# Optimization experiments

Hardware: AMD Instinct MI355X
Metric: run time of the kernel (lower is better)

## Reference

```python
import jax, jax.numpy as jnp
import numpy as np

XY = 16   # xy_size
Z = 16    # z_size
S = XY * XY * Z   # num_states = 4096
V = 2048  # num_tokens


def _build_structure():
    # Static 3D-grid neighbor structure (replaces the per-state Python loop).
    h = np.arange(S)
    zc, rem = np.divmod(h, XY * XY)
    yc, xc = np.divmod(rem, XY)
    coords = np.stack([xc, yc, zc], 1)                       # [S,3] (x,y,z)
    offs = np.array([[0, 0, 0], [1, 0, 0], [-1, 0, 0], [0, 1, 0],
                     [0, -1, 0], [0, 0, 1], [0, 0, 2]])       # 7 fixed offsets
    nc = coords[:, None, :] + offs[None]                      # [S,7,3]
    valid = ((nc[..., 0] >= 0) & (nc[..., 0] < XY) &
             (nc[..., 1] >= 0) & (nc[..., 1] < XY) &
             (nc[..., 2] >= 0) & (nc[..., 2] < Z))
    dest = nc[..., 0] + XY * (nc[..., 1] + XY * nc[..., 2])   # flat neighbor idx
    # compact valid neighbors to the front, preserving offset order:
    # j-th valid neighbor consumes logit j (matches logits[h, :len(valid)])
    order = np.argsort(~valid, axis=1, kind='stable')
    tgt = np.take_along_axis(dest, order, axis=1)
    vmask = np.take_along_axis(valid, order, axis=1)
    tgt = np.where(vmask, tgt, S)  # invalid slots -> dummy column S
    return jnp.asarray(tgt), jnp.asarray(vmask)

TGT, VMASK = _build_structure()


def transition_log_p(trans_w):
    # masked log-softmax over the first k valid logits of each row
    logits = jnp.where(VMASK, trans_w, -1e30)
    logp = jax.nn.log_softmax(logits, axis=1)
    logp = jnp.where(VMASK, logp, -jnp.inf)
    T = jnp.full((S, S + 1), -jnp.inf, trans_w.dtype)
    T = T.at[jnp.arange(S)[:, None], TGT].set(logp)
    return T[:, :S]  # [S,S], row h = log p(transition targets of h)


def smoothed_emission(emis_w):
    em = jax.nn.log_softmax(emis_w, axis=-1).reshape(Z, XY, XY, V)
    lv, rv = em[:, :, :1], em[:, :, -1:]
    lh, rh = em[:, :1], em[:, -1:]
    c = jnp.zeros((Z, 1, 1, V), em.dtype)  # log(1)=0 pad, as in the original
    c2 = lambda *a: jnp.concatenate(a, axis=2)
    c1 = lambda *a: jnp.concatenate(a, axis=1)
    up = c1(c2(lv, em, rv), c2(c, rh, c), c2(c, rh, c))
    dn = c1(c2(c, lh, c), c2(c, lh, c), c2(lv, em, rv))
    lf = c1(c2(lh, c, c), c2(em, rv, rv), c2(rh, c, c))
    rt = c1(c2(c, c, lh), c2(lv, lv, em), c2(c, c, rh))
    cr = c1(c2(c, lh, c), c2(lv, em, rv), c2(c, rh, c))
    mean = jax.nn.logsumexp(jnp.stack((up, dn, lf, rt, cr)), axis=0) - jnp.log(5.0)
    return mean[:, 1:-1, 1:-1].reshape(S, V)


def _forward(stories, trans_w, emis_w, prior_w):
    priors = jax.nn.log_softmax(prior_w)                      # [S]
    em = smoothed_emission(emis_w)                            # [S,V]
    padded = jnp.concatenate([em, jnp.zeros((S, 1), em.dtype)], axis=1)  # [S,V+1]
    # per-(story, step) emission log-prob: sum over sentence tokens
    all_emis = padded.T[stories].sum(axis=2)                  # [B,L,S]
    all_emis = jnp.transpose(all_emis, (1, 0, 2))             # [L,B,S]
    T = transition_log_p(trans_w)                             # [S,S]
    amax = jnp.max(T, axis=1, keepdims=True)                  # [S,1], finite (self-loop)
    P = jnp.exp(T - amax)                                     # [S,S]
    score0 = all_emis[0] + priors                             # [B,S]

    def step(score, em_t):
        # new[b,a] = em_t[b,a] + logsumexp_h(T[a,h] + score[b,h])  (stable log-matmul)
        smax = jnp.max(score, axis=1, keepdims=True)          # [B,1]
        new = em_t + jnp.log(jnp.exp(score - smax) @ P.T) + smax + amax.T
        return new, new

    _, rest = jax.lax.scan(step, score0, all_emis[1:])
    return jnp.concatenate([score0[None], rest], axis=0)      # [L,B,S]


def setup_inputs() -> dict:
    key = jax.random.key(0)
    k1, k2, k3, k4 = jax.random.split(key, 4)
    B, L, W = 8, 32, 8
    return {
        "stories_tensor": jax.random.randint(k1, (B, L, W), 0, V + 1, dtype=jnp.int32),
        "story_length": L,
        "trans_w": jax.random.normal(k2, (S, 7), jnp.float32),
        "emis_w": jax.random.normal(k3, (S, V), jnp.float32),
        "prior_w": jax.random.normal(k4, (S,), jnp.float32),
    }


def reference(stories_tensor, story_length, trans_w, emis_w, prior_w):
    assert stories_tensor.shape[1] == story_length
    return _forward(stories_tensor, trans_w, emis_w, prior_w)
```

## Files before the change

kernel.cpp:

```cpp
#include <hip/hip_runtime.h>
#include <math.h>

#define XYD 16
#define ZD 16
#define SS 4096
#define VV 2048
#define BB 8
#define LL 32
#define WW 8
#define VC 32
#define SM_STRIDE 257

#define GUARD_L 16
#define GUARD_R 512
#define EBUF_N (GUARD_L + SS + GUARD_R)

__global__ void k_logZ(const float* __restrict__ emis_w, float* __restrict__ logZ) {
    int wave = threadIdx.x >> 6;
    int lane = threadIdx.x & 63;
    int row  = blockIdx.x * 4 + wave;
    const float* r = emis_w + (size_t)row * VV;
    float vals[32];
    float m = -INFINITY;
#pragma unroll
    for (int k = 0; k < 8; k++) {
        float4 f = ((const float4*)r)[k * 64 + lane];
        vals[k*4+0] = f.x; vals[k*4+1] = f.y; vals[k*4+2] = f.z; vals[k*4+3] = f.w;
    }
#pragma unroll
    for (int k = 0; k < 32; k++) m = fmaxf(m, vals[k]);
#pragma unroll
    for (int o = 32; o; o >>= 1) m = fmaxf(m, __shfl_xor(m, o));
    float sum = 0.f;
#pragma unroll
    for (int k = 0; k < 32; k++) sum += __expf(vals[k] - m);
#pragma unroll
    for (int o = 32; o; o >>= 1) sum += __shfl_xor(sum, o);
    if (lane == 0) logZ[row] = m + __logf(sum);
}

__global__ void k_smooth(const float* __restrict__ emis_w, const float* __restrict__ logZ,
                         float* __restrict__ smT) {
    __shared__ float tileT[VC * SM_STRIDE];
    int z  = blockIdx.x;
    int v0 = blockIdx.y * VC;
    int tid = threadIdx.x;
    int rsub = tid >> 3;
    int c0   = (tid & 7) * 4;

#pragma unroll
    for (int it = 0; it < 8; it++) {
        int r  = it * 32 + rsub;
        int sg = z * 256 + r;
        float lz = logZ[sg];
        float4 w = *(const float4*)(emis_w + (size_t)sg * VV + v0 + c0);
        tileT[(c0+0)*SM_STRIDE + r] = __expf(w.x - lz);
        tileT[(c0+1)*SM_STRIDE + r] = __expf(w.y - lz);
        tileT[(c0+2)*SM_STRIDE + r] = __expf(w.z - lz);
        tileT[(c0+3)*SM_STRIDE + r] = __expf(w.w - lz);
    }
    __syncthreads();

    int x = tid & 15, y = tid >> 4;
    int sxp = (x < 15) ? tid + 1  : tid;
    int sxm = (x > 0)  ? tid - 1  : tid;
    int syp = (y < 15) ? tid + 16 : tid;
    int sym = (y > 0)  ? tid - 16 : tid;
    float* o = smT + (size_t)v0 * SS + z * 256 + tid;
#pragma unroll
    for (int i = 0; i < VC; i++) {
        const float* tb = tileT + i * SM_STRIDE;
        float s = tb[tid] + tb[sxp] + tb[sxm] + tb[syp] + tb[sym];
        o[(size_t)i * SS] = __logf(s * 0.2f);
    }
}

__global__ void k_emis(const int* __restrict__ stories, const float* __restrict__ smT,
                       float* __restrict__ all_emis) {
    int blk = blockIdx.x;
    int t = blk >> 3, b = blk & 7;
    int tid = threadIdx.x;
    int tok[WW];
#pragma unroll
    for (int w = 0; w < WW; w++) tok[w] = stories[(b * LL + t) * WW + w];
#pragma unroll
    for (int i = 0; i < 4; i++) {
        int s = i * 1024 + tid * 4;
        float4 acc = {0.f, 0.f, 0.f, 0.f};
#pragma unroll
        for (int w = 0; w < WW; w++) {
            if (tok[w] < VV) {
                float4 f = *(const float4*)(smT + (size_t)tok[w] * SS + s);
                acc.x += f.x; acc.y += f.y; acc.z += f.z; acc.w += f.w;
            }
        }
        *(float4*)(all_emis + ((size_t)t * BB + b) * SS + s) = acc;
    }
}

__global__ void __launch_bounds__(1024) k_forward(
    const float* __restrict__ trans_w, const float* __restrict__ prior_w,
    const float* __restrict__ all_emis, float* __restrict__ out) {
    __shared__ __align__(16) float Ebuf[2][EBUF_N];
    __shared__ float red2[2][20];
    __shared__ float pr[16];
    int b = blockIdx.x;
    int tid = threadIdx.x;
    int lane = tid & 63, wid = tid >> 6;

    if (tid < GUARD_L) { Ebuf[0][tid] = 0.f; Ebuf[1][tid] = 0.f; }
    if (tid < GUARD_R) {
        Ebuf[0][GUARD_L + SS + tid] = 0.f;
        Ebuf[1][GUARD_L + SS + tid] = 0.f;
    }
    if (tid < 2) {
        red2[tid][0]  = -INFINITY; red2[tid][17] = -INFINITY;
        red2[tid][18] = -INFINITY; red2[tid][19] = -INFINITY;
    }

    float pw[28], am[4];
    {
        float w7[28];
        const float4* t4 = (const float4*)(trans_w + (size_t)tid * 28);
#pragma unroll
        for (int k = 0; k < 7; k++) ((float4*)w7)[k] = t4[k];
#pragma unroll
        for (int i = 0; i < 4; i++) {
            int j = tid * 4 + i;
            int xx = j & 15, yy = (j >> 4) & 15, zz = j >> 8;
            bool val[7];
            val[0] = true;
            val[1] = (xx < 15); val[2] = (xx > 0);
            val[3] = (yy < 15); val[4] = (yy > 0);
            val[5] = (zz < 15); val[6] = (zz < 14);
            const float* rw = w7 + i * 7;
            float w[7]; int cnt = 0; float m = -INFINITY;
#pragma unroll
            for (int d = 0; d < 7; d++) { if (val[d]) { w[d] = rw[cnt++]; m = fmaxf(m, w[d]); } }
            float se = 0.f;
#pragma unroll
            for (int d = 0; d < 7; d++) if (val[d]) se += __expf(w[d] - m);
#pragma unroll
            for (int d = 0; d < 7; d++) pw[i*7+d] = val[d] ? __expf(w[d] - m) : 0.f;
            am[i] = -__logf(se);
        }
    }

    float4 pv = ((const float4*)prior_w)[tid];
    float4 em = ((const float4*)(all_emis + (size_t)b * SS))[tid];

    float lm = fmaxf(fmaxf(pv.x, pv.y), fmaxf(pv.z, pv.w));
#pragma unroll
    for (int o = 32; o; o >>= 1) lm = fmaxf(lm, __shfl_xor(lm, o));
    if (lane == 0) pr[wid] = lm;
    __syncthreads();
    float gm = pr[0];
#pragma unroll
    for (int w = 1; w < 16; w++) gm = fmaxf(gm, pr[w]);
    __syncthreads();
    float ls = __expf(pv.x - gm) + __expf(pv.y - gm) + __expf(pv.z - gm) + __expf(pv.w - gm);
#pragma unroll
    for (int o = 32; o; o >>= 1) ls += __shfl_xor(ls, o);
    if (lane == 0) pr[wid] = ls;
    __syncthreads();
    float gs = 0.f;
#pragma unroll
    for (int w = 0; w < 16; w++) gs += pr[w];
    float logZp = gm + __logf(gs);

    float v0 = em.x + pv.x - logZp;
    float v1 = em.y + pv.y - logZp;
    float v2 = em.z + pv.z - logZp;
    float v3 = em.w + pv.w - logZp;
    { float4 ov = {v0, v1, v2, v3}; ((float4*)(out + (size_t)b * SS))[tid] = ov; }
    float c = fmaxf(fmaxf(v0, v1), fmaxf(v2, v3));
#pragma unroll
    for (int o = 32; o; o >>= 1) c = fmaxf(c, __shfl_xor(c, o));
    float4 Ereg;
    Ereg.x = __expf(v0 - c); Ereg.y = __expf(v1 - c);
    Ereg.z = __expf(v2 - c); Ereg.w = __expf(v3 - c);
    ((float4*)(Ebuf[0] + GUARD_L))[tid] = Ereg;
    if (lane == 0) red2[0][1 + wid] = c;

    float4 em_next = ((const float4*)(all_emis + (size_t)BB * SS + (size_t)b * SS))[tid];

    int cur = 0;
    for (int t = 1; t < LL; t++) {
        __syncthreads();
        em = em_next;
        if (t < LL - 1)
            em_next = ((const float4*)(all_emis + ((size_t)(t + 1) * BB + b) * SS))[tid];

        const float* rr = red2[cur];
        float c_m1 = rr[wid], c0f = rr[wid + 1], c1f = rr[wid + 2], c2f = rr[wid + 3];
        bool lo = (lane < 4);
        float X = fmaxf(fmaxf(c0f, c1f), c2f);
        if (lo) X = fmaxf(X, c_m1);
        float f0 = __expf(c0f - X), f1 = __expf(c1f - X), f2 = __expf(c2f - X);
        float fm1 = lo ? __expf(c_m1 - X) : 0.f;

        const float*  Es = Ebuf[cur] + GUARD_L;
        const float4* Ep = (const float4*)Es;
        float  bx  = Es[4 * tid + 4];
        float  cxw = Es[4 * tid - 1];
        float4 Yp = Ep[tid + 4];
        float4 Ym = Ep[tid - 4];
        float4 Zp = Ep[tid + 64];
        float4 Zq = Ep[tid + 128];

        float4 Af;
        Af.x = Ereg.x * f0; Af.y = Ereg.y * f0; Af.z = Ereg.z * f0; Af.w = Ereg.w * f0;
        bx  *= (lane == 63) ? f1 : f0;
        cxw *= (lane == 0)  ? fm1 : f0;
        float fyp = (lane >= 60) ? f1 : f0;
        float fym = lo ? fm1 : f0;
        Yp.x *= fyp; Yp.y *= fyp; Yp.z *= fyp; Yp.w *= fyp;
        Ym.x *= fym; Ym.y *= fym; Ym.z *= fym; Ym.w *= fym;
        Zp.x *= f1;  Zp.y *= f1;  Zp.z *= f1;  Zp.w *= f1;
        Zq.x *= f2;  Zq.y *= f2;  Zq.z *= f2;  Zq.w *= f2;

        float a0 = Af.x*pw[0]  + Af.y*pw[1]  + cxw*pw[2]   + Yp.x*pw[3]  + Ym.x*pw[4]  + Zp.x*pw[5]  + Zq.x*pw[6];
        float a1 = Af.y*pw[7]  + Af.z*pw[8]  + Af.x*pw[9]  + Yp.y*pw[10] + Ym.y*pw[11] + Zp.y*pw[12] + Zq.y*pw[13];
        float a2 = Af.z*pw[14] + Af.w*pw[15] + Af.y*pw[16] + Yp.z*pw[17] + Ym.z*pw[18] + Zp.z*pw[19] + Zq.z*pw[20];
        float a3 = Af.w*pw[21] + bx*pw[22]   + Af.z*pw[23] + Yp.w*pw[24] + Ym.w*pw[25] + Zp.w*pw[26] + Zq.w*pw[27];

        v0 = em.x + __logf(a0) + X + am[0];
        v1 = em.y + __logf(a1) + X + am[1];
        v2 = em.z + __logf(a2) + X + am[2];
        v3 = em.w + __logf(a3) + X + am[3];

        { float4 ov = {v0, v1, v2, v3};
          ((float4*)(out + ((size_t)t * BB + b) * SS))[tid] = ov; }

        c = fmaxf(fmaxf(v0, v1), fmaxf(v2, v3));
#pragma unroll
        for (int o = 32; o; o >>= 1) c = fmaxf(c, __shfl_xor(c, o));
        Ereg.x = __expf(v0 - c); Ereg.y = __expf(v1 - c);
        Ereg.z = __expf(v2 - c); Ereg.w = __expf(v3 - c);
        ((float4*)(Ebuf[cur ^ 1] + GUARD_L))[tid] = Ereg;
        if (lane == 0) red2[cur ^ 1][1 + wid] = c;

        cur ^= 1;
    }
}

extern "C" void kernel_launch(void* const* d_in, const int* in_sizes, int n_in,
                              void* d_out, int out_size, void* d_ws, size_t ws_size,
                              hipStream_t stream) {
    const int*   stories = (const int*)d_in[0];
    const float* trans_w = (const float*)d_in[2];
    const float* emis_w  = (const float*)d_in[3];
    const float* prior_w = (const float*)d_in[4];
    float* out = (float*)d_out;

    char* ws = (char*)d_ws;
    float* smT      = (float*)(ws);
    float* all_emis = (float*)(ws + (size_t)VV * SS * 4);
    float* logZ     = (float*)(ws + (size_t)VV * SS * 4 + (size_t)LL * BB * SS * 4);

    k_logZ<<<SS / 4, 256, 0, stream>>>(emis_w, logZ);
    k_smooth<<<dim3(ZD, VV / VC), 256, 0, stream>>>(emis_w, logZ, smT);
    k_emis<<<LL * BB, 256, 0, stream>>>(stories, smT, all_emis);
    k_forward<<<BB, 1024, 0, stream>>>(trans_w, prior_w, all_emis, out);
}
```

Measured before the change: 167.1 us.

## Store forward exp-buffer in bf16 and replace per-wave max with extrapolated shift

The recursion's shared exp buffer now holds bf16 values instead of fp32, which halves LDS traffic for the stencil neighbour loads. The per-wave max reduction (shuffles plus cross-wave rescale factors) is dropped. Each step instead uses a single scalar shift: state 0's score, linearly extrapolated from the previous two steps. This removes several shuffles, exps and multiplies from the serial per-step critical path. The costs are bf16 truncation error and possible overflow or underflow of exp when other states drift far from state 0's score.

```diff
diff --git a/kernel.cpp b/kernel.cpp
--- a/kernel.cpp
+++ b/kernel.cpp
@@ -15,6 +15,13 @@
 #define GUARD_R 512
 #define EBUF_N (GUARD_L + SS + GUARD_R)
 
+__device__ __forceinline__ float b2f(unsigned short u) {
+    union { unsigned int i; float f; } x; x.i = ((unsigned int)u) << 16; return x.f;
+}
+__device__ __forceinline__ unsigned short f2b(float f) {
+    union { float f; unsigned int i; } x; x.f = f; return (unsigned short)(x.i >> 16);
+}
+
 __global__ void k_logZ(const float* __restrict__ emis_w, float* __restrict__ logZ) {
     int wave = threadIdx.x >> 6;
     int lane = threadIdx.x & 63;
@@ -101,21 +108,17 @@
 __global__ void __launch_bounds__(1024) k_forward(
     const float* __restrict__ trans_w, const float* __restrict__ prior_w,
     const float* __restrict__ all_emis, float* __restrict__ out) {
-    __shared__ __align__(16) float Ebuf[2][EBUF_N];
-    __shared__ float red2[2][20];
+    __shared__ __align__(16) unsigned short Ebuf[2][EBUF_N];
+    __shared__ float red2[2];
     __shared__ float pr[16];
     int b = blockIdx.x;
     int tid = threadIdx.x;
     int lane = tid & 63, wid = tid >> 6;
 
-    if (tid < GUARD_L) { Ebuf[0][tid] = 0.f; Ebuf[1][tid] = 0.f; }
+    if (tid < GUARD_L) { Ebuf[0][tid] = 0; Ebuf[1][tid] = 0; }
     if (tid < GUARD_R) {
-        Ebuf[0][GUARD_L + SS + tid] = 0.f;
-        Ebuf[1][GUARD_L + SS + tid] = 0.f;
-    }
-    if (tid < 2) {
-        red2[tid][0]  = -INFINITY; red2[tid][17] = -INFINITY;
-        red2[tid][18] = -INFINITY; red2[tid][19] = -INFINITY;
+        Ebuf[0][GUARD_L + SS + tid] = 0;
+        Ebuf[1][GUARD_L + SS + tid] = 0;
     }
 
     float pw[28], am[4];
@@ -173,14 +176,18 @@
     float v2 = em.z + pv.z - logZp;
     float v3 = em.w + pv.w - logZp;
     { float4 ov = {v0, v1, v2, v3}; ((float4*)(out + (size_t)b * SS))[tid] = ov; }
-    float c = fmaxf(fmaxf(v0, v1), fmaxf(v2, v3));
-#pragma unroll
-    for (int o = 32; o; o >>= 1) c = fmaxf(c, __shfl_xor(c, o));
-    float4 Ereg;
-    Ereg.x = __expf(v0 - c); Ereg.y = __expf(v1 - c);
-    Ereg.z = __expf(v2 - c); Ereg.w = __expf(v3 - c);
-    ((float4*)(Ebuf[0] + GUARD_L))[tid] = Ereg;
-    if (lane == 0) red2[0][1 + wid] = c;
+    if (tid == 0) red2[0] = v0;
+    __syncthreads();
+    float g1 = red2[0];
+    float XpPrev = g1;
+    {
+        ushort4 E;
+        E.x = f2b(__expf(v0 - XpPrev)); E.y = f2b(__expf(v1 - XpPrev));
+        E.z = f2b(__expf(v2 - XpPrev)); E.w = f2b(__expf(v3 - XpPrev));
+        *(ushort4*)(&Ebuf[0][GUARD_L + 4 * tid]) = E;
+    }
+    float Erx = __expf(v0 - XpPrev), Ery = __expf(v1 - XpPrev);
+    float Erz = __expf(v2 - XpPrev), Erw = __expf(v3 - XpPrev);
 
     float4 em_next = ((const float4*)(all_emis + (size_t)BB * SS + (size_t)b * SS))[tid];
 
@@ -191,56 +198,40 @@
         if (t < LL - 1)
             em_next = ((const float4*)(all_emis + ((size_t)(t + 1) * BB + b) * SS))[tid];
 
-        const float* rr = red2[cur];
-        float c_m1 = rr[wid], c0f = rr[wid + 1], c1f = rr[wid + 2], c2f = rr[wid + 3];
-        bool lo = (lane < 4);
-        float X = fmaxf(fmaxf(c0f, c1f), c2f);
-        if (lo) X = fmaxf(X, c_m1);
-        float f0 = __expf(c0f - X), f1 = __expf(c1f - X), f2 = __expf(c2f - X);
-        float fm1 = lo ? __expf(c_m1 - X) : 0.f;
-
-        const float*  Es = Ebuf[cur] + GUARD_L;
-        const float4* Ep = (const float4*)Es;
-        float  bx  = Es[4 * tid + 4];
-        float  cxw = Es[4 * tid - 1];
-        float4 Yp = Ep[tid + 4];
-        float4 Ym = Ep[tid - 4];
-        float4 Zp = Ep[tid + 64];
-        float4 Zq = Ep[tid + 128];
-
-        float4 Af;
-        Af.x = Ereg.x * f0; Af.y = Ereg.y * f0; Af.z = Ereg.z * f0; Af.w = Ereg.w * f0;
-        bx  *= (lane == 63) ? f1 : f0;
-        cxw *= (lane == 0)  ? fm1 : f0;
-        float fyp = (lane >= 60) ? f1 : f0;
-        float fym = lo ? fm1 : f0;
-        Yp.x *= fyp; Yp.y *= fyp; Yp.z *= fyp; Yp.w *= fyp;
-        Ym.x *= fym; Ym.y *= fym; Ym.z *= fym; Ym.w *= fym;
-        Zp.x *= f1;  Zp.y *= f1;  Zp.z *= f1;  Zp.w *= f1;
-        Zq.x *= f2;  Zq.y *= f2;  Zq.z *= f2;  Zq.w *= f2;
-
-        float a0 = Af.x*pw[0]  + Af.y*pw[1]  + cxw*pw[2]   + Yp.x*pw[3]  + Ym.x*pw[4]  + Zp.x*pw[5]  + Zq.x*pw[6];
-        float a1 = Af.y*pw[7]  + Af.z*pw[8]  + Af.x*pw[9]  + Yp.y*pw[10] + Ym.y*pw[11] + Zp.y*pw[12] + Zq.y*pw[13];
-        float a2 = Af.z*pw[14] + Af.w*pw[15] + Af.y*pw[16] + Yp.z*pw[17] + Ym.z*pw[18] + Zp.z*pw[19] + Zq.z*pw[20];
-        float a3 = Af.w*pw[21] + bx*pw[22]   + Af.z*pw[23] + Yp.w*pw[24] + Ym.w*pw[25] + Zp.w*pw[26] + Zq.w*pw[27];
-
-        v0 = em.x + __logf(a0) + X + am[0];
-        v1 = em.y + __logf(a1) + X + am[1];
-        v2 = em.z + __logf(a2) + X + am[2];
-        v3 = em.w + __logf(a3) + X + am[3];
+        float g0 = red2[cur];
+        float Xp = 2.f * g0 - g1;
+
+        const unsigned short* Eb = Ebuf[cur] + GUARD_L + 4 * tid;
+        ushort4 YpU = *(const ushort4*)(Eb + 16);
+        ushort4 YmU = *(const ushort4*)(Eb - 16);
+        ushort4 ZpU = *(const ushort4*)(Eb + 256);
+        ushort4 ZqU = *(const ushort4*)(Eb + 512);
+        float bx  = b2f(Eb[4]);
+        float cxw = b2f(Eb[-1]);
+
+        float a0 = Erx*pw[0]  + Ery*pw[1]  + cxw*pw[2]        + b2f(YpU.x)*pw[3]  + b2f(YmU.x)*pw[4]  + b2f(ZpU.x)*pw[5]  + b2f(ZqU.x)*pw[6];
+        float a1 = Ery*pw[7]  + Erz*pw[8]  + Erx*pw[9]        + b2f(YpU.y)*pw[10] + b2f(YmU.y)*pw[11] + b2f(ZpU.y)*pw[12] + b2f(ZqU.y)*pw[13];
+        float a2 = Erz*pw[14] + Erw*pw[15] + Ery*pw[16]       + b2f(YpU.z)*pw[17] + b2f(YmU.z)*pw[18] + b2f(ZpU.z)*pw[19] + b2f(ZqU.z)*pw[20];
+        float a3 = Erw*pw[21] + bx*pw[22]  + Erz*pw[23]       + b2f(YpU.w)*pw[24] + b2f(YmU.w)*pw[25] + b2f(ZpU.w)*pw[26] + b2f(ZqU.w)*pw[27];
+
+        v0 = em.x + __logf(a0) + XpPrev + am[0];
+        v1 = em.y + __logf(a1) + XpPrev + am[1];
+        v2 = em.z + __logf(a2) + XpPrev + am[2];
+        v3 = em.w + __logf(a3) + XpPrev + am[3];
 
         { float4 ov = {v0, v1, v2, v3};
           ((float4*)(out + ((size_t)t * BB + b) * SS))[tid] = ov; }
 
-        c = fmaxf(fmaxf(v0, v1), fmaxf(v2, v3));
-#pragma unroll
-        for (int o = 32; o; o >>= 1) c = fmaxf(c, __shfl_xor(c, o));
-        Ereg.x = __expf(v0 - c); Ereg.y = __expf(v1 - c);
-        Ereg.z = __expf(v2 - c); Ereg.w = __expf(v3 - c);
-        ((float4*)(Ebuf[cur ^ 1] + GUARD_L))[tid] = Ereg;
-        if (lane == 0) red2[cur ^ 1][1 + wid] = c;
-
-        cur ^= 1;
+        Erx = __expf(v0 - Xp); Ery = __expf(v1 - Xp);
+        Erz = __expf(v2 - Xp); Erw = __expf(v3 - Xp);
+        {
+            ushort4 E;
+            E.x = f2b(Erx); E.y = f2b(Ery); E.z = f2b(Erz); E.w = f2b(Erw);
+            *(ushort4*)(&Ebuf[cur ^ 1][GUARD_L + 4 * tid]) = E;
+        }
+        if (tid == 0) red2[cur ^ 1] = v0;
+
+        g1 = g0; XpPrev = Xp; cur ^= 1;
     }
 }
 
```

Measured after the change: 156.6 us. 6.3% less time.
